# Kernel tuning notes

Hardware: AMD Instinct MI355X
Metric: run time of the kernel (lower is better)

Reference implementation:

```python
import jax, jax.numpy as jnp
import numpy as np

NFEAT, NHID = 128, 128

def setup_inputs() -> dict:
    key = jax.random.key(0)
    k1, k2, k3, k4 = jax.random.split(key, 4)
    x = jax.random.normal(k1, (32, 1024, NFEAT), dtype=jnp.float32)
    adj = jax.random.uniform(k2, (32, 1024, 1024), dtype=jnp.float32)
    # GraphConvolution parameters (Kipf init ~ uniform, scale irrelevant for correctness)
    bound = 1.0 / np.sqrt(NHID)
    W = jax.random.uniform(k3, (NFEAT, NHID), dtype=jnp.float32, minval=-bound, maxval=bound)
    b = jax.random.uniform(k4, (NHID,), dtype=jnp.float32, minval=-bound, maxval=bound)
    return {"x": x, "adj": adj, "W": W, "b": b}

def reference(x, adj, W, b):
    # Batched equivalent of the per-sample python loop:
    # out[i] = relu(adj[i] @ (x[i] @ W) + b); dropout is identity in eval mode.
    support = jnp.einsum('bnf,fh->bnh', x, W)          # [B, N, nhid]
    out = jnp.einsum('bnm,bmh->bnh', adj, support) + b  # [B, N, nhid]
    return jax.nn.relu(out)
```

## Files before the change

kernel.cpp:

```cpp
#include <hip/hip_runtime.h>
#include <stdint.h>


typedef short bf16x8 __attribute__((ext_vector_type(8)));
typedef float f32x4 __attribute__((ext_vector_type(4)));
typedef unsigned short u16x8 __attribute__((ext_vector_type(8)));

__device__ __forceinline__ unsigned short f2bf(float f) {
    uint32_t u = __builtin_bit_cast(uint32_t, f);
    u += 0x7FFFu + ((u >> 16) & 1u);
    return (unsigned short)(u >> 16);
}

__device__ __forceinline__ bf16x8 cvt8(f32x4 v0, f32x4 v1) {
    u16x8 p;
    p[0] = f2bf(v0.x); p[1] = f2bf(v0.y); p[2] = f2bf(v0.z); p[3] = f2bf(v0.w);
    p[4] = f2bf(v1.x); p[5] = f2bf(v1.y); p[6] = f2bf(v1.z); p[7] = f2bf(v1.w);
    return __builtin_bit_cast(bf16x8, p);
}

__global__ __launch_bounds__(256) void k0_wt(const float* __restrict__ W,
                                             unsigned short* __restrict__ WT) {
    int o = blockIdx.x * 256 + threadIdx.x;
    int h = o >> 7, f = o & 127;
    WT[o] = f2bf(W[f * 128 + h]);
}

__global__ __launch_bounds__(256) void k1_support(const float* __restrict__ x,
                                                  const unsigned short* __restrict__ WT,
                                                  unsigned short* __restrict__ ST) {
    int t = threadIdx.x;
    int wv = t >> 6, lane = t & 63, l16 = lane & 15, quad = lane >> 4;
    int wave_h = (wv & 1) * 64, wave_m = (wv >> 1) * 32;
    int node_base = blockIdx.x * 64;
    const float* xb = x + (size_t)node_base * 128;

    f32x4 acc[4][2];
#pragma unroll
    for (int ht = 0; ht < 4; ++ht)
#pragma unroll
        for (int mt = 0; mt < 2; ++mt) acc[ht][mt] = 0.f;

#pragma unroll
    for (int s = 0; s < 4; ++s) {
        int ko = s * 32 + quad * 8;
        bf16x8 a[4], bb[2];
#pragma unroll
        for (int ht = 0; ht < 4; ++ht)
            a[ht] = *(const bf16x8*)&WT[(wave_h + ht * 16 + l16) * 128 + ko];
#pragma unroll
        for (int mt = 0; mt < 2; ++mt) {
            const float* xr = xb + (size_t)(wave_m + mt * 16 + l16) * 128 + ko;
            bb[mt] = cvt8(*(const f32x4*)xr, *(const f32x4*)(xr + 4));
        }
#pragma unroll
        for (int ht = 0; ht < 4; ++ht)
#pragma unroll
            for (int mt = 0; mt < 2; ++mt)
                acc[ht][mt] = __builtin_amdgcn_mfma_f32_16x16x32_bf16(
                    a[ht], bb[mt], acc[ht][mt], 0, 0, 0);
    }

    int batch = blockIdx.x >> 4;
    int m_in_b = (blockIdx.x & 15) * 64;
#pragma unroll
    for (int ht = 0; ht < 4; ++ht)
#pragma unroll
        for (int mt = 0; mt < 2; ++mt) {
            int mcol = wave_m + mt * 16 + l16;
#pragma unroll
            for (int r = 0; r < 4; ++r) {
                int h = wave_h + ht * 16 + quad * 4 + r;
                ST[(((size_t)batch * 128 + h) << 10) + m_in_b + mcol] =
                    f2bf(acc[ht][mt][r]);
            }
        }
}

__global__ __launch_bounds__(256) void k2_gcn(const float* __restrict__ adj,
                                              const unsigned short* __restrict__ ST,
                                              const float* __restrict__ bias,
                                              float* __restrict__ out) {
    int t = threadIdx.x;
    int batch = blockIdx.x >> 4;
    int mbase = (blockIdx.x & 15) * 64;
    int wv = t >> 6, lane = t & 63, l16 = lane & 15, quad = lane >> 4;
    int wave_m = (wv & 1) * 32, wave_n = (wv >> 1) * 64;

    float bv[4];
#pragma unroll
    for (int j = 0; j < 4; ++j) bv[j] = bias[wave_n + j * 16 + l16];

    f32x4 acc[2][4];
#pragma unroll
    for (int i = 0; i < 2; ++i)
#pragma unroll
        for (int j = 0; j < 4; ++j) acc[i][j] = 0.f;

    const float* adjb = adj + ((size_t)batch * 1024 + mbase) * 1024;
    const unsigned short* stb = ST + ((size_t)batch * 128) * 1024;

    for (int kb = 0; kb < 16; ++kb) {
#pragma unroll
        for (int s = 0; s < 2; ++s) {
            int ko = kb * 64 + s * 32 + quad * 8;
            bf16x8 a[2], bb[4];
#pragma unroll
            for (int i = 0; i < 2; ++i) {
                const float* ar = adjb + (size_t)(wave_m + i * 16 + l16) * 1024 + ko;
                a[i] = cvt8(*(const f32x4*)ar, *(const f32x4*)(ar + 4));
            }
#pragma unroll
            for (int j = 0; j < 4; ++j)
                bb[j] = *(const bf16x8*)&stb[(size_t)(wave_n + j * 16 + l16) * 1024 + ko];
#pragma unroll
            for (int i = 0; i < 2; ++i)
#pragma unroll
                for (int j = 0; j < 4; ++j)
                    acc[i][j] = __builtin_amdgcn_mfma_f32_16x16x32_bf16(
                        a[i], bb[j], acc[i][j], 0, 0, 0);
        }
    }

    float* outb = out + ((size_t)batch * 1024 + mbase) * 128;
#pragma unroll
    for (int i = 0; i < 2; ++i)
#pragma unroll
        for (int j = 0; j < 4; ++j) {
            int n = wave_n + j * 16 + l16;
#pragma unroll
            for (int r = 0; r < 4; ++r) {
                int m = wave_m + i * 16 + quad * 4 + r;
                float v = acc[i][j][r] + bv[j];
                outb[(size_t)m * 128 + n] = fmaxf(v, 0.f);
            }
        }
}

extern "C" void kernel_launch(void* const* d_in, const int* in_sizes, int n_in,
                              void* d_out, int out_size, void* d_ws, size_t ws_size,
                              hipStream_t stream) {
    const float* x = (const float*)d_in[0];
    const float* adj = (const float*)d_in[1];
    const float* W = (const float*)d_in[2];
    const float* b = (const float*)d_in[3];
    float* out = (float*)d_out;

    unsigned short* ST = (unsigned short*)d_ws;
    unsigned short* WT = (unsigned short*)d_ws + (size_t)32 * 128 * 1024;

    k0_wt<<<64, 256, 0, stream>>>(W, WT);
    k1_support<<<512, 256, 0, stream>>>(x, WT, ST);
    k2_gcn<<<512, 256, 0, stream>>>(adj, ST, b, out);
}
```

Baseline: 247.5 us.

## Double-buffer adj and support tiles in LDS via async global-to-LDS loads

The GCN aggregation kernel now stages adj (fp32) and support (bf16) tiles into swizzled, double-buffered shared memory with global_load_lds, prefetching the next K block while MFMAs run on the current one. Blocks are also remapped so neighbouring block IDs land on different batches, and launch bounds request two blocks per CU. This targets memory latency from the direct per-lane global loads. In exchange it uses about 64KB of LDS per block and adds a barrier each iteration, which can limit occupancy.

```diff
diff --git a/kernel.cpp b/kernel.cpp
--- a/kernel.cpp
+++ b/kernel.cpp
@@ -18,6 +18,11 @@
     p[4] = f2bf(v1.x); p[5] = f2bf(v1.y); p[6] = f2bf(v1.z); p[7] = f2bf(v1.w);
     return __builtin_bit_cast(bf16x8, p);
 }
+
+#define GLD16(g, l)                                                         \
+    __builtin_amdgcn_global_load_lds(                                       \
+        (const __attribute__((address_space(1))) unsigned int*)(g),         \
+        (__attribute__((address_space(3))) unsigned int*)(l), 16, 0, 0)
 
 __global__ __launch_bounds__(256) void k0_wt(const float* __restrict__ W,
                                              unsigned short* __restrict__ WT) {
@@ -77,15 +82,27 @@
         }
 }
 
-__global__ __launch_bounds__(256) void k2_gcn(const float* __restrict__ adj,
-                                              const unsigned short* __restrict__ ST,
-                                              const float* __restrict__ bias,
-                                              float* __restrict__ out) {
+__global__ __launch_bounds__(256, 2) void k2_gcn(const float* __restrict__ adj,
+                                                 const unsigned short* __restrict__ ST,
+                                                 const float* __restrict__ bias,
+                                                 float* __restrict__ out) {
+    __shared__ __align__(16) unsigned char As[2][64 * 256];
+    __shared__ __align__(16) unsigned char Bs[2][128 * 128];
     int t = threadIdx.x;
-    int batch = blockIdx.x >> 4;
-    int mbase = (blockIdx.x & 15) * 64;
+    int bid = (int)blockIdx.x;
+    int orig = (bid & 7) * 64 + (bid >> 3);
+    int batch = orig >> 4;
+    int mbase = (orig & 15) * 64;
     int wv = t >> 6, lane = t & 63, l16 = lane & 15, quad = lane >> 4;
     int wave_m = (wv & 1) * 32, wave_n = (wv >> 1) * 64;
+
+    const char* adjB = (const char*)(adj + ((size_t)batch * 1024 + mbase) * 1024);
+    const char* stB  = (const char*)(ST + ((size_t)batch * 128) * 1024);
+
+    int cA = (t & 15) ^ ((t >> 4) & 7);
+    const char* srcA0 = adjB + (size_t)(t >> 4) * 4096 + cA * 16;
+    int cB = (t & 7) ^ ((t >> 3) & 7);
+    const char* srcB0 = stB + (size_t)(t >> 3) * 2048 + cB * 16;
 
     float bv[4];
 #pragma unroll
@@ -97,29 +114,55 @@
 #pragma unroll
         for (int j = 0; j < 4; ++j) acc[i][j] = 0.f;
 
-    const float* adjb = adj + ((size_t)batch * 1024 + mbase) * 1024;
-    const unsigned short* stb = ST + ((size_t)batch * 128) * 1024;
+    int aswz = l16 & 7;
+    int arow = (wave_m + l16) * 256;
+    int brow = (wave_n + l16) * 128;
 
-    for (int kb = 0; kb < 16; ++kb) {
+    auto STAGE = [&](int buf, int kb) {
+        char* dA = (char*)As[buf] + t * 16;
+        const char* sA = srcA0 + kb * 256;
+#pragma unroll
+        for (int i = 0; i < 4; ++i) GLD16(sA + i * 65536, dA + i * 4096);
+        char* dB = (char*)Bs[buf] + t * 16;
+        const char* sB = srcB0 + kb * 128;
+#pragma unroll
+        for (int i = 0; i < 4; ++i) GLD16(sB + i * 65536, dB + i * 4096);
+    };
+
+    auto COMPUTE = [&](int buf) {
 #pragma unroll
         for (int s = 0; s < 2; ++s) {
-            int ko = kb * 64 + s * 32 + quad * 8;
-            bf16x8 a[2], bb[4];
+            bf16x8 afr[2];
 #pragma unroll
-            for (int i = 0; i < 2; ++i) {
-                const float* ar = adjb + (size_t)(wave_m + i * 16 + l16) * 1024 + ko;
-                a[i] = cvt8(*(const f32x4*)ar, *(const f32x4*)(ar + 4));
+            for (int im = 0; im < 2; ++im) {
+                int c0 = (s * 8 + quad * 2) ^ aswz;
+                int c1 = c0 ^ 1;
+                f32x4 lo = *(const f32x4*)(As[buf] + arow + im * 4096 + c0 * 16);
+                f32x4 hi = *(const f32x4*)(As[buf] + arow + im * 4096 + c1 * 16);
+                afr[im] = cvt8(lo, hi);
+            }
+            bf16x8 bfr[4];
+#pragma unroll
+            for (int j = 0; j < 4; ++j) {
+                int c = (s * 4 + quad) ^ aswz;
+                bfr[j] = *(const bf16x8*)(Bs[buf] + brow + j * 2048 + c * 16);
             }
 #pragma unroll
-            for (int j = 0; j < 4; ++j)
-                bb[j] = *(const bf16x8*)&stb[(size_t)(wave_n + j * 16 + l16) * 1024 + ko];
-#pragma unroll
-            for (int i = 0; i < 2; ++i)
+            for (int im = 0; im < 2; ++im)
 #pragma unroll
                 for (int j = 0; j < 4; ++j)
-                    acc[i][j] = __builtin_amdgcn_mfma_f32_16x16x32_bf16(
-                        a[i], bb[j], acc[i][j], 0, 0, 0);
+                    acc[im][j] = __builtin_amdgcn_mfma_f32_16x16x32_bf16(
+                        afr[im], bfr[j], acc[im][j], 0, 0, 0);
         }
+    };
+
+    STAGE(0, 0);
+    __syncthreads();
+    for (int kb = 0; kb < 16; ++kb) {
+        int cur = kb & 1;
+        if (kb < 15) STAGE(cur ^ 1, kb + 1);
+        COMPUTE(cur);
+        if (kb < 15) __syncthreads();
     }
 
     float* outb = out + ((size_t)batch * 1024 + mbase) * 128;
```

New measurement: 229.2 us. -7.4%, faster.

## Stage adj and support tiles through LDS with a 4-deep async pipeline

Applied to the files above, without the earlier changes.

The GCN aggregation kernel now copies adj and support tiles from global memory straight into LDS with global_load_lds, using four buffers and keeping three stages in flight, guarded by vmcnt waits and barriers. Before, each wave issued direct global loads and waited on them inside the MFMA loop. The aim is to hide memory latency on the large fp32 adj stream. Block indices are also remapped so that neighbouring blocks touch different batches, and launch bounds request two blocks per CU. The cost is 64 KB of LDS per block, which limits occupancy, and hand-written waitcnt and sched_barrier logic that depends on an exact count of outstanding loads.

```diff
diff --git a/kernel.cpp b/kernel.cpp
--- a/kernel.cpp
+++ b/kernel.cpp
@@ -18,6 +18,11 @@
     p[4] = f2bf(v1.x); p[5] = f2bf(v1.y); p[6] = f2bf(v1.z); p[7] = f2bf(v1.w);
     return __builtin_bit_cast(bf16x8, p);
 }
+
+#define GLD16(g, l)                                                         \
+    __builtin_amdgcn_global_load_lds(                                       \
+        (const __attribute__((address_space(1))) unsigned int*)(g),         \
+        (__attribute__((address_space(3))) unsigned int*)(l), 16, 0, 0)
 
 __global__ __launch_bounds__(256) void k0_wt(const float* __restrict__ W,
                                              unsigned short* __restrict__ WT) {
@@ -77,16 +82,32 @@
         }
 }
 
-__global__ __launch_bounds__(256) void k2_gcn(const float* __restrict__ adj,
-                                              const unsigned short* __restrict__ ST,
-                                              const float* __restrict__ bias,
-                                              float* __restrict__ out) {
+__global__ __launch_bounds__(256, 2) void k2_gcn(const float* __restrict__ adj,
+                                                 const unsigned short* __restrict__ ST,
+                                                 const float* __restrict__ bias,
+                                                 float* __restrict__ out) {
+    __shared__ __align__(16) char As[4][8192];
+    __shared__ __align__(16) char Bs[4][8192];
     int t = threadIdx.x;
-    int batch = blockIdx.x >> 4;
-    int mbase = (blockIdx.x & 15) * 64;
+    int bid = (int)blockIdx.x;
+    int orig = (bid & 7) * 64 + (bid >> 3);
+    int batch = orig >> 4;
+    int mbase = (orig & 15) * 64;
     int wv = t >> 6, lane = t & 63, l16 = lane & 15, quad = lane >> 4;
     int wave_m = (wv & 1) * 32, wave_n = (wv >> 1) * 64;
 
+    const char* adjB = (const char*)(adj + ((size_t)batch * 1024 + mbase) * 1024);
+    const char* stB  = (const char*)(ST + ((size_t)batch * 128) * 1024);
+
+    const char* sA[2];
+    const char* sB[2];
+#pragma unroll
+    for (int i = 0; i < 2; ++i) {
+        int o = i * 256 + t;
+        sA[i] = adjB + (size_t)(o & 63) * 4096 + (o >> 6) * 16;
+        sB[i] = stB + (size_t)(o & 127) * 2048 + (o >> 7) * 16;
+    }
+
     float bv[4];
 #pragma unroll
     for (int j = 0; j < 4; ++j) bv[j] = bias[wave_n + j * 16 + l16];
@@ -97,30 +118,58 @@
 #pragma unroll
         for (int j = 0; j < 4; ++j) acc[i][j] = 0.f;
 
-    const float* adjb = adj + ((size_t)batch * 1024 + mbase) * 1024;
-    const unsigned short* stb = ST + ((size_t)batch * 128) * 1024;
-
-    for (int kb = 0; kb < 16; ++kb) {
-#pragma unroll
-        for (int s = 0; s < 2; ++s) {
-            int ko = kb * 64 + s * 32 + quad * 8;
-            bf16x8 a[2], bb[4];
-#pragma unroll
-            for (int i = 0; i < 2; ++i) {
-                const float* ar = adjb + (size_t)(wave_m + i * 16 + l16) * 1024 + ko;
-                a[i] = cvt8(*(const f32x4*)ar, *(const f32x4*)(ar + 4));
-            }
+    auto STAGE = [&](int kb) {
+        int buf = kb & 3;
+        char* dA = &As[buf][t * 16];
+        char* dB = &Bs[buf][t * 16];
+#pragma unroll
+        for (int i = 0; i < 2; ++i) GLD16(sA[i] + kb * 128, dA + i * 4096);
+#pragma unroll
+        for (int i = 0; i < 2; ++i) GLD16(sB[i] + kb * 64, dB + i * 4096);
+    };
+
+    auto COMPUTE = [&](int kb) {
+        int buf = kb & 3;
+        const char* A = As[buf];
+        const char* B = Bs[buf];
+        bf16x8 afr[2], bfr[4];
+#pragma unroll
+        for (int im = 0; im < 2; ++im) {
+            int row = wave_m + im * 16 + l16;
+            f32x4 lo = *(const f32x4*)(A + ((2 * quad) * 64 + row) * 16);
+            f32x4 hi = *(const f32x4*)(A + ((2 * quad + 1) * 64 + row) * 16);
+            afr[im] = cvt8(lo, hi);
+        }
+#pragma unroll
+        for (int j = 0; j < 4; ++j)
+            bfr[j] = *(const bf16x8*)(B + (quad * 128 + wave_n + j * 16 + l16) * 16);
+#pragma unroll
+        for (int im = 0; im < 2; ++im)
 #pragma unroll
             for (int j = 0; j < 4; ++j)
-                bb[j] = *(const bf16x8*)&stb[(size_t)(wave_n + j * 16 + l16) * 1024 + ko];
-#pragma unroll
-            for (int i = 0; i < 2; ++i)
-#pragma unroll
-                for (int j = 0; j < 4; ++j)
-                    acc[i][j] = __builtin_amdgcn_mfma_f32_16x16x32_bf16(
-                        a[i], bb[j], acc[i][j], 0, 0, 0);
-        }
+                acc[im][j] = __builtin_amdgcn_mfma_f32_16x16x32_bf16(
+                    afr[im], bfr[j], acc[im][j], 0, 0, 0);
+    };
+
+    STAGE(0);
+    STAGE(1);
+    STAGE(2);
+    for (int kb = 0; kb < 30; ++kb) {
+        asm volatile("s_waitcnt vmcnt(8)");
+        __builtin_amdgcn_s_barrier();
+        __builtin_amdgcn_sched_barrier(0);
+        COMPUTE(kb);
+        if (kb < 29) STAGE(kb + 3);
+        __builtin_amdgcn_sched_barrier(0);
     }
+    asm volatile("s_waitcnt vmcnt(4)");
+    __builtin_amdgcn_s_barrier();
+    __builtin_amdgcn_sched_barrier(0);
+    COMPUTE(30);
+    asm volatile("s_waitcnt vmcnt(0)");
+    __builtin_amdgcn_s_barrier();
+    __builtin_amdgcn_sched_barrier(0);
+    COMPUTE(31);
 
     float* outb = out + ((size_t)batch * 1024 + mbase) * 128;
 #pragma unroll
```

New measurement: 238.5 us. 1.04x faster.
